# Optimization experiments

Measured on AMD Instinct MI355X. Metric: run time of the kernel, lower is better.

Reference implementation:

```python
import jax, jax.numpy as jnp
import numpy as np

B, T, NE, NZ, H = 64, 1024, 256, 64, 256  # batch, timesteps, n_e, n_z, encoder_hidden
SW_HID = 128  # switch MLP hidden width (hardcoded in source)


def setup_inputs() -> dict:
    key = jax.random.key(0)
    ks = jax.random.split(key, 16)
    s = 0.05
    p = lambda k, shape: (jax.random.normal(k, shape, dtype=jnp.float32) * s)
    return {
        "e_seq": jax.random.normal(ks[0], (B, T, NE), dtype=jnp.float32),
        "eps": jax.random.normal(ks[1], (B, T, NZ), dtype=jnp.float32),  # randn_like noise, precomputed
        # GRU forward direction (torch layout: weight_ih [3H, NE] order r,z,n)
        "w_ih_f": p(ks[2], (3 * H, NE)), "w_hh_f": p(ks[3], (3 * H, H)),
        "b_ih_f": jnp.zeros((3 * H,), jnp.float32), "b_hh_f": jnp.zeros((3 * H,), jnp.float32),
        # GRU backward direction
        "w_ih_b": p(ks[4], (3 * H, NE)), "w_hh_b": p(ks[5], (3 * H, H)),
        "b_ih_b": jnp.zeros((3 * H,), jnp.float32), "b_hh_b": jnp.zeros((3 * H,), jnp.float32),
        # mu / logvar heads over [B,T,2H]
        "mu_w": p(ks[6], (NZ, 2 * H)), "mu_b": jnp.zeros((NZ,), jnp.float32),
        "lv_w": p(ks[7], (NZ, 2 * H)), "lv_b": jnp.zeros((NZ,), jnp.float32),
        # switching unit: Linear(NE + 2H + NZ, 128) -> ReLU -> Linear(128,1) -> Sigmoid
        "sw_w1": p(ks[8], (SW_HID, NE + 2 * H + NZ)), "sw_b1": jnp.zeros((SW_HID,), jnp.float32),
        "sw_w2": p(ks[9], (1, SW_HID)), "sw_b2": jnp.zeros((1,), jnp.float32),
    }


def _gru_dir(x, w_ih, w_hh, b_ih, b_hh, reverse):
    # x: [B,T,NE]; torch GRU cell: r,z = sigmoid; n = tanh(x_n + r*(W_hn h + b_hn)); h' = (1-z)*n + z*h
    xp = jnp.einsum('btn,gn->btg', x, w_ih) + b_ih  # [B,T,3H] input projections, once
    xp = jnp.swapaxes(xp, 0, 1)  # [T,B,3H]
    h0 = jnp.zeros((x.shape[0], w_hh.shape[1]), x.dtype)

    def step(h, xpt):
        hp = h @ w_hh.T + b_hh
        xr, xz, xn = jnp.split(xpt, 3, axis=-1)
        hr, hz, hn = jnp.split(hp, 3, axis=-1)
        r = jax.nn.sigmoid(xr + hr)
        z = jax.nn.sigmoid(xz + hz)
        n = jnp.tanh(xn + r * hn)
        h_new = (1.0 - z) * n + z * h
        return h_new, h_new

    _, hs = jax.lax.scan(step, h0, xp, reverse=reverse)  # outputs time-aligned even when reversed
    return jnp.swapaxes(hs, 0, 1)  # [B,T,H]


def _forward(e_seq, eps, w_ih_f, w_hh_f, b_ih_f, b_hh_f, w_ih_b, w_hh_b, b_ih_b, b_hh_b,
             mu_w, mu_b, lv_w, lv_b, sw_w1, sw_b1, sw_w2, sw_b2):
    h_f = _gru_dir(e_seq, w_ih_f, w_hh_f, b_ih_f, b_hh_f, reverse=False)
    h_b = _gru_dir(e_seq, w_ih_b, w_hh_b, b_ih_b, b_hh_b, reverse=True)
    h_seq = jnp.concatenate([h_f, h_b], axis=-1)  # [B,T,2H]

    mu = h_seq @ mu_w.T + mu_b    # [B,T,NZ]
    lv = h_seq @ lv_w.T + lv_b    # [B,T,NZ]

    n_e = e_seq.shape[-1]
    h2 = h_seq.shape[-1]
    # split switch first-layer weight by input segments [e_t | h_t | z_prev]
    w1_e = sw_w1[:, :n_e]
    w1_h = sw_w1[:, n_e:n_e + h2]
    w1_z = sw_w1[:, n_e + h2:]
    # precompute e/h contributions for all t; only z_prev contribution is sequential
    pre = jnp.einsum('btn,kn->btk', e_seq, w1_e) + jnp.einsum('bth,kh->btk', h_seq, w1_h) + sw_b1  # [B,T,128]

    z_tilde = mu + jnp.exp(0.5 * lv) * eps                    # reparameterized sample [B,T,NZ]
    kl = (-0.5 * (1.0 + lv - mu * mu - jnp.exp(lv))).sum(-1)  # [B,T]

    def step(z_prev, inputs):
        pre_t, zt_t = inputs  # [B,128], [B,NZ]
        hid = jax.nn.relu(pre_t + z_prev @ w1_z.T)
        beta = jax.nn.sigmoid(hid @ sw_w2.T + sw_b2)[..., 0]  # [B]
        z_t = beta[:, None] * zt_t + (1.0 - beta[:, None]) * z_prev
        return z_t, (z_t, beta)

    z0 = jnp.zeros((e_seq.shape[0], mu.shape[-1]), e_seq.dtype)
    _, (zs, betas) = jax.lax.scan(step, z0, (jnp.swapaxes(pre, 0, 1), jnp.swapaxes(z_tilde, 0, 1)))
    z_seq = jnp.swapaxes(zs, 0, 1)     # [B,T,NZ]
    beta_seq = jnp.swapaxes(betas, 0, 1)  # [B,T]
    kl_loss = kl.mean()
    return z_seq, kl_loss, beta_seq


def reference(e_seq, eps, w_ih_f, w_hh_f, b_ih_f, b_hh_f, w_ih_b, w_hh_b, b_ih_b, b_hh_b,
              mu_w, mu_b, lv_w, lv_b, sw_w1, sw_b1, sw_w2, sw_b2):
    return _forward(e_seq, eps, w_ih_f, w_hh_f, b_ih_f, b_hh_f, w_ih_b, w_hh_b, b_ih_b, b_hh_b,
                    mu_w, mu_b, lv_w, lv_b, sw_w1, sw_b1, sw_w2, sw_b2)
```

## Files before the change

kernel.cpp:

```cpp
#include <hip/hip_runtime.h>
#include <cstdint>

typedef _Float16 half_t;
typedef _Float16 half2_t __attribute__((ext_vector_type(2)));
typedef _Float16 h8_t __attribute__((ext_vector_type(8)));
typedef float f4_t __attribute__((ext_vector_type(4)));
typedef unsigned int uint32;
typedef uint32 uv16 __attribute__((ext_vector_type(16)));

static constexpr int B_ = 64, T_ = 1024;

#define DEV __device__ __forceinline__

DEV float fdot2f(half2_t a, half2_t b, float c) {
#if __has_builtin(__builtin_amdgcn_fdot2)
  return __builtin_amdgcn_fdot2(a, b, c, false);
#else
  return fmaf((float)a.x, (float)b.x, fmaf((float)a.y, (float)b.y, c));
#endif
}

DEV float fast_rcp(float x) { return __builtin_amdgcn_rcpf(x); }
DEV float sigmf(float x) { return fast_rcp(1.f + __expf(-x)); }
DEV float tanhf_(float x) { return 1.f - 2.f * fast_rcp(1.f + __expf(2.f * x)); }
DEV uint32 pack2(float a, float b) {
  half2_t h; h.x = (half_t)a; h.y = (half_t)b;
  return __builtin_bit_cast(uint32, h);
}
DEV half2_t bch2(uint32 u) { return __builtin_bit_cast(half2_t, u); }

DEV void gload_lds16(const void* g, void* l) {
  __builtin_amdgcn_global_load_lds(
      (const __attribute__((address_space(1))) uint32*)g,
      (__attribute__((address_space(3))) uint32*)l, 16, 0, 0);
}

#define WSEL(va, vb, j) bch2(((j) < 16) ? (va)[(j) & 15] : (vb)[((j) - 16) & 15])

__global__ __launch_bounds__(256) void pack_w(
    const float* __restrict__ w_ih_f, const float* __restrict__ w_ih_b,
    const float* __restrict__ mu_w, const float* __restrict__ lv_w,
    const float* __restrict__ sw_w1,
    const float* __restrict__ w_hh_f, const float* __restrict__ w_hh_b,
    const float* __restrict__ b_ih_f, const float* __restrict__ b_ih_b,
    const float* __restrict__ b_hh_f, const float* __restrict__ b_hh_b,
    const float* __restrict__ mu_b, const float* __restrict__ lv_b,
    const float* __restrict__ sw_b1,
    uint32* __restrict__ wihf, uint32* __restrict__ wihb,
    uint32* __restrict__ wchf, uint32* __restrict__ wchb, uint32* __restrict__ wce2,
    uint32* __restrict__ whh, uint32* __restrict__ w1z,
    float* __restrict__ biasc, float* __restrict__ biasf, float* __restrict__ biasb) {
  int id = blockIdx.x * 256 + threadIdx.x;
  if (id < 98304) { wihf[id] = pack2(w_ih_f[2*id], w_ih_f[2*id+1]); return; }
  id -= 98304;
  if (id < 98304) { wihb[id] = pack2(w_ih_b[2*id], w_ih_b[2*id+1]); return; }
  id -= 98304;
  if (id < 32768) {
    int n = id >> 7, c0 = (id & 127) * 2;
    const float* p = (n < 64)  ? mu_w + n * 512 + c0
                   : (n < 128) ? lv_w + (n - 64) * 512 + c0
                               : sw_w1 + (n - 128) * 832 + 256 + c0;
    wchf[id] = pack2(p[0], p[1]); return;
  }
  id -= 32768;
  if (id < 32768) {
    int n = id >> 7, c0 = (id & 127) * 2;
    const float* p = (n < 64)  ? mu_w + n * 512 + 256 + c0
                   : (n < 128) ? lv_w + (n - 64) * 512 + 256 + c0
                               : sw_w1 + (n - 128) * 832 + 512 + c0;
    wchb[id] = pack2(p[0], p[1]); return;
  }
  id -= 32768;
  if (id < 16384) {
    int n = id >> 7, c0 = (id & 127) * 2;
    wce2[id] = pack2(sw_w1[n * 832 + c0], sw_w1[n * 832 + c0 + 1]); return;
  }
  id -= 16384;
  if (id < 196608) {
    int dd = id / 98304, q = id % 98304;
    int j = q >> 9, t2 = q & 511;
    int rr = t2 >> 2, pp = t2 & 3;
    int gi = j >> 5, ck = j & 31;
    int g = gi >> 1, i = gi & 1;
    int row = 256 * g + 2 * rr + i;
    int k0 = pp * 64 + 2 * ck;
    const float* w = dd ? w_hh_b : w_hh_f;
    whh[id] = pack2(w[row * 256 + k0], w[row * 256 + k0 + 1]);
    return;
  }
  id -= 196608;
  if (id < 4096) {
    int j = id >> 6, kk = id & 63;
    int row = (j < 32) ? kk : kk + 64;
    int jj = j & 31;
    w1z[id] = pack2(sw_w1[row * 832 + 768 + 2 * jj], sw_w1[row * 832 + 768 + 2 * jj + 1]);
    return;
  }
  id -= 4096;
  if (id < 256) {
    biasc[id] = (id < 64) ? mu_b[id] : (id < 128) ? lv_b[id - 64] : sw_b1[id - 128];
    return;
  }
  id -= 256;
  if (id < 768) { biasf[id] = b_ih_f[id] + (id < 512 ? b_hh_f[id] : 0.f); return; }
  id -= 768;
  if (id < 768) { biasb[id] = b_ih_b[id] + (id < 512 ? b_hh_b[id] : 0.f); return; }
}

template <int AF32, int ACC>
__global__ __launch_bounds__(256) void gemm_t(
    const void* __restrict__ Ap, int lda,
    const half_t* __restrict__ Bw,
    const float* __restrict__ bias,
    half_t* __restrict__ C, int ldc, int K) {
  __shared__ __align__(16) half_t smem[16384];
  half_t* As = smem;
  half_t* Bs = smem + 8192;
  const int tid = threadIdx.x;
  const int lane = tid & 63, w = tid >> 6;
  const int n0 = blockIdx.x * 128, m0 = blockIdx.y * 128;
  const int r8 = lane >> 3, c8 = lane & 7;
  f4_t acc[4][4];
  f4_t zero = {0.f, 0.f, 0.f, 0.f};
#pragma unroll
  for (int i = 0; i < 4; ++i)
#pragma unroll
    for (int j = 0; j < 4; ++j) acc[i][j] = zero;
  const int wm = (w >> 1) * 64, wn = (w & 1) * 64;
  for (int ks = 0; ks < K; ks += 64) {
    if constexpr (AF32) {
      const float* Af = (const float*)Ap;
#pragma unroll
      for (int it = 0; it < 4; ++it) {
        int c = it * 256 + tid;
        int row = c >> 3, coff = (c & 7) * 8;
        const float* ap = Af + (size_t)(m0 + row) * lda + ks + coff;
        float4 v0 = *(const float4*)ap;
        float4 v1 = *(const float4*)(ap + 4);
        uint4 u;
        u.x = pack2(v0.x, v0.y); u.y = pack2(v0.z, v0.w);
        u.z = pack2(v1.x, v1.y); u.w = pack2(v1.z, v1.w);
        *(uint4*)&As[(size_t)c * 8] = u;
      }
    } else {
      const half_t* Af = (const half_t*)Ap;
#pragma unroll
      for (int c = 0; c < 4; ++c) {
        int row = w * 32 + c * 8 + r8;
        gload_lds16(Af + (size_t)(m0 + row) * lda + ks + c8 * 8, As + (w * 4 + c) * 512);
      }
    }
#pragma unroll
    for (int c = 0; c < 4; ++c) {
      int row = w * 32 + c * 8 + r8;
      gload_lds16(Bw + (size_t)(n0 + row) * K + ks + c8 * 8, Bs + (w * 4 + c) * 512);
    }
    __syncthreads();
#pragma unroll
    for (int kk = 0; kk < 2; ++kk) {
      h8_t af[4], bf[4];
      const int ko = kk * 32 + (lane >> 4) * 8;
#pragma unroll
      for (int i = 0; i < 4; ++i) af[i] = *(const h8_t*)&As[(wm + i * 16 + (lane & 15)) * 64 + ko];
#pragma unroll
      for (int j = 0; j < 4; ++j) bf[j] = *(const h8_t*)&Bs[(wn + j * 16 + (lane & 15)) * 64 + ko];
#pragma unroll
      for (int i = 0; i < 4; ++i)
#pragma unroll
        for (int j = 0; j < 4; ++j)
          acc[i][j] = __builtin_amdgcn_mfma_f32_16x16x32_f16(af[i], bf[j], acc[i][j], 0, 0, 0);
    }
    __syncthreads();
  }
  const int cl4 = lane & 15, rl4 = lane >> 4;
#pragma unroll
  for (int j = 0; j < 4; ++j) {
    float bj = bias ? bias[n0 + wn + j * 16 + cl4] : 0.f;
#pragma unroll
    for (int i = 0; i < 4; ++i)
#pragma unroll
      for (int q = 0; q < 4; ++q) {
        int rl = wm + i * 16 + rl4 * 4 + q;
        int cc = wn + j * 16 + cl4;
        smem[rl * 128 + cc] = (half_t)(acc[i][j][q] + bj);
      }
  }
  __syncthreads();
#pragma unroll
  for (int it = 0; it < 8; ++it) {
    int idx = it * 256 + tid;
    int row = idx >> 4, colc = idx & 15;
    uint4 v = *(const uint4*)&smem[row * 128 + colc * 8];
    half_t* cp = C + (size_t)(m0 + row) * ldc + n0 + colc * 8;
    if constexpr (ACC) {
      uint4 o = *(const uint4*)cp;
      h8_t vv = __builtin_bit_cast(h8_t, v) + __builtin_bit_cast(h8_t, o);
      v = __builtin_bit_cast(uint4, vv);
    }
    *(uint4*)cp = v;
  }
}

__global__ __launch_bounds__(512, 2) void gru_rec(
    uint32* __restrict__ xp,
    const uint32* __restrict__ whh2,
    const float* __restrict__ bhh_f, const float* __restrict__ bhh_b) {
  const int wg = blockIdx.x;
  const int d = wg >> 6, b = wg & 63;
  const int tid = threadIdx.x;
  const int r = tid >> 2, p = tid & 3;
  __shared__ uint32 hb[2][144];
  if (tid < 144) { hb[0][tid] = 0; hb[1][tid] = 0; }
  uv16 w0a, w0b, w1a, w1b, w2a, w2b, w3a, w3b, w4a, w4b, w5a, w5b;
  {
    const uint32* wp = whh2 + (size_t)d * 98304 + tid;
#define LD16(vec, base)                                   \
  _Pragma("unroll") for (int e = 0; e < 16; ++e) vec[e] = \
      wp[(size_t)((base) + e) * 512];
    LD16(w0a, 0);   LD16(w0b, 16);  LD16(w1a, 32);  LD16(w1b, 48);
    LD16(w2a, 64);  LD16(w2b, 80);  LD16(w3a, 96);  LD16(w3b, 112);
    LD16(w4a, 128); LD16(w4b, 144); LD16(w5a, 160); LD16(w5b, 176);
#undef LD16
    asm volatile("" : "+v"(w0a), "+v"(w0b), "+v"(w1a), "+v"(w1b), "+v"(w2a), "+v"(w2b));
    asm volatile("" : "+v"(w3a), "+v"(w3b), "+v"(w4a), "+v"(w4b), "+v"(w5a), "+v"(w5b));
  }
  const float* bhh = d ? bhh_b : bhh_f;
  const float bhn0 = bhh[512 + 2 * r], bhn1 = bhh[512 + 2 * r + 1];
  uint32* xpu = xp + ((size_t)d * B_ + b) * T_ * 384;
  float h0 = 0.f, h1 = 0.f;
  const int dt = d ? -1 : 1;
  int t = d ? (T_ - 1) : 0;
  uint32 xr_n = 0, xz_n = 0, xn_n = 0;
  if (p == 0) {
    const uint32* rowp = xpu + (size_t)t * 384;
    xr_n = rowp[r]; xz_n = rowp[128 + r]; xn_n = rowp[256 + r];
  }
  const int rdbase = p * 36;
  const int wslice = (r >> 5) * 36 + (r & 31);
  __syncthreads();
  for (int step = 0; step < T_; ++step) {
    const int cur = step & 1;
    const uint32 xr = xr_n, xz = xz_n, xn = xn_n;
    const int tn = (step < T_ - 1) ? (t + dt) : t;
    if (p == 0) {
      const uint32* rowp = xpu + (size_t)tn * 384;
      xr_n = rowp[r]; xz_n = rowp[128 + r]; xn_n = rowp[256 + r];
    }
    float a00 = 0, a10 = 0, a01 = 0, a11 = 0, a02 = 0, a12 = 0;
    const uint32* hc = &hb[cur][rdbase];
#pragma unroll
    for (int c = 0; c < 4; ++c) {
      uint4 u0 = *(const uint4*)(hc + c * 8);
      uint4 u1 = *(const uint4*)(hc + c * 8 + 4);
      uint32 hv[8] = {u0.x, u0.y, u0.z, u0.w, u1.x, u1.y, u1.z, u1.w};
#pragma unroll
      for (int e = 0; e < 8; ++e) {
        const int j = c * 8 + e;
        half2_t hh = bch2(hv[e]);
        a00 = fdot2f(WSEL(w0a, w0b, j), hh, a00);
        a10 = fdot2f(WSEL(w1a, w1b, j), hh, a10);
        a01 = fdot2f(WSEL(w2a, w2b, j), hh, a01);
        a11 = fdot2f(WSEL(w3a, w3b, j), hh, a11);
        a02 = fdot2f(WSEL(w4a, w4b, j), hh, a02);
        a12 = fdot2f(WSEL(w5a, w5b, j), hh, a12);
      }
    }
    a00 += __shfl_xor(a00, 1); a00 += __shfl_xor(a00, 2);
    a10 += __shfl_xor(a10, 1); a10 += __shfl_xor(a10, 2);
    a01 += __shfl_xor(a01, 1); a01 += __shfl_xor(a01, 2);
    a11 += __shfl_xor(a11, 1); a11 += __shfl_xor(a11, 2);
    a02 += __shfl_xor(a02, 1); a02 += __shfl_xor(a02, 2);
    a12 += __shfl_xor(a12, 1); a12 += __shfl_xor(a12, 2);
    if (p == 0) {
      half2_t xrv = bch2(xr), xzv = bch2(xz), xnv = bch2(xn);
      float r0 = sigmf((float)xrv.x + a00);
      float z0 = sigmf((float)xzv.x + a01);
      float n0 = tanhf_((float)xnv.x + r0 * (a02 + bhn0));
      h0 = (1.f - z0) * n0 + z0 * h0;
      float r1 = sigmf((float)xrv.y + a10);
      float z1 = sigmf((float)xzv.y + a11);
      float n1 = tanhf_((float)xnv.y + r1 * (a12 + bhn1));
      h1 = (1.f - z1) * n1 + z1 * h1;
      uint32 ph = pack2(h0, h1);
      hb[cur ^ 1][wslice] = ph;
      xpu[(size_t)t * 384 + r] = ph;
    }
    __syncthreads();
    t = tn;
  }
}

__global__ __launch_bounds__(256) void zkl(const half_t* __restrict__ hp,
                                           const float* __restrict__ eps,
                                           float* __restrict__ ztil,
                                           float* __restrict__ klp) {
  const int blk = blockIdx.x, tid = threadIdx.x;
  const size_t bt = (size_t)blk * 4 + (tid >> 6);
  const int j = tid & 63;
  float mu = (float)hp[bt * 768 + j];
  float lv = (float)hp[bt * 768 + 64 + j];
  float ev = eps[bt * 64 + j];
  ztil[bt * 64 + j] = mu + __expf(0.5f * lv) * ev;
  float term = 1.f + lv - mu * mu - __expf(lv);
#pragma unroll
  for (int s = 1; s < 64; s <<= 1) term += __shfl_xor(term, s);
  __shared__ float red[4];
  if ((tid & 63) == 0) red[tid >> 6] = term;
  __syncthreads();
  if (tid == 0) klp[blk] = red[0] + red[1] + red[2] + red[3];
}

__global__ __launch_bounds__(256) void klred(const float* __restrict__ klp,
                                             float* __restrict__ out) {
  const int tid = threadIdx.x;
  float s = 0.f;
  for (int i = tid; i < 16384; i += 256) s += klp[i];
#pragma unroll
  for (int st = 1; st < 64; st <<= 1) s += __shfl_xor(s, st);
  __shared__ float red[4];
  if ((tid & 63) == 0) red[tid >> 6] = s;
  __syncthreads();
  if (tid == 0) out[0] = (red[0] + red[1] + red[2] + red[3]) * (-0.5f / 65536.f);
}

__global__ __launch_bounds__(64) void z_scan(
    const half_t* __restrict__ hp,
    const float* __restrict__ zt_arr,
    const uint32* __restrict__ w1z,
    const float* __restrict__ sw_w2, const float* __restrict__ sw_b2,
    float* __restrict__ z_out, float* __restrict__ beta_out) {
  const int b = blockIdx.x;
  const int k = threadIdx.x;
  uv16 z0a, z0b, z1a, z1b;
  {
#define LDZ(vec, base)                                    \
  _Pragma("unroll") for (int e = 0; e < 16; ++e) vec[e] = \
      w1z[((base) + e) * 64 + k];
    LDZ(z0a, 0); LDZ(z0b, 16); LDZ(z1a, 32); LDZ(z1b, 48);
#undef LDZ
    asm volatile("" : "+v"(z0a), "+v"(z0b), "+v"(z1a), "+v"(z1b));
  }
  const float w2k0 = sw_w2[k], w2k1 = sw_w2[k + 64], b2 = sw_b2[0];
  __shared__ uint32 zbuf[2][32];
  if (k < 32) { zbuf[0][k] = 0; zbuf[1][k] = 0; }
  __syncthreads();
  float zf = 0.f;
  const size_t bt0 = (size_t)b * T_;
  float pre0n = (float)hp[bt0 * 768 + 128 + k];
  float pre1n = (float)hp[bt0 * 768 + 192 + k];
  float ztn = zt_arr[bt0 * 64 + k];
  for (int t = 0; t < T_; ++t) {
    const int cur = t & 1;
    const float pre0 = pre0n, pre1 = pre1n, zt = ztn;
    const int tn = (t < T_ - 1) ? t + 1 : t;
    pre0n = (float)hp[(bt0 + tn) * 768 + 128 + k];
    pre1n = (float)hp[(bt0 + tn) * 768 + 192 + k];
    ztn = zt_arr[(bt0 + tn) * 64 + k];
    float a0 = 0, a1 = 0, a2 = 0, a3 = 0;
#pragma unroll
    for (int q = 0; q < 8; ++q) {
      uint4 u = *(const uint4*)&zbuf[cur][q * 4];
      const int m = q * 4;
      a0 = fdot2f(WSEL(z0a, z0b, m),     bch2(u.x), a0);
      a1 = fdot2f(WSEL(z0a, z0b, m + 1), bch2(u.y), a1);
      a0 = fdot2f(WSEL(z0a, z0b, m + 2), bch2(u.z), a0);
      a1 = fdot2f(WSEL(z0a, z0b, m + 3), bch2(u.w), a1);
      a2 = fdot2f(WSEL(z1a, z1b, m),     bch2(u.x), a2);
      a3 = fdot2f(WSEL(z1a, z1b, m + 1), bch2(u.y), a3);
      a2 = fdot2f(WSEL(z1a, z1b, m + 2), bch2(u.z), a2);
      a3 = fdot2f(WSEL(z1a, z1b, m + 3), bch2(u.w), a3);
    }
    float hid0 = fmaxf(pre0 + a0 + a1, 0.f);
    float hid1 = fmaxf(pre1 + a2 + a3, 0.f);
    float v = fmaf(hid0, w2k0, hid1 * w2k1);
#pragma unroll
    for (int s = 1; s < 64; s <<= 1) v += __shfl_xor(v, s);
    const float beta = sigmf(v + b2);
    zf = beta * zt + (1.f - beta) * zf;
    z_out[(bt0 + t) * 64 + k] = zf;
    if (k == 0) beta_out[bt0 + t] = beta;
    float zo = __shfl_xor(zf, 1);
    if ((k & 1) == 0) zbuf[cur ^ 1][k >> 1] = pack2(zf, zo);
    asm volatile("s_waitcnt lgkmcnt(0)" ::: "memory");
  }
}

extern "C" void kernel_launch(void* const* d_in, const int* in_sizes, int n_in,
                              void* d_out, int out_size, void* d_ws, size_t ws_size,
                              hipStream_t stream) {
  (void)in_sizes; (void)n_in; (void)out_size;
  const float* e_seq  = (const float*)d_in[0];
  const float* eps    = (const float*)d_in[1];
  const float* w_ih_f = (const float*)d_in[2];
  const float* w_hh_f = (const float*)d_in[3];
  const float* b_ih_f = (const float*)d_in[4];
  const float* b_hh_f = (const float*)d_in[5];
  const float* w_ih_b = (const float*)d_in[6];
  const float* w_hh_b = (const float*)d_in[7];
  const float* b_ih_b = (const float*)d_in[8];
  const float* b_hh_b = (const float*)d_in[9];
  const float* mu_w   = (const float*)d_in[10];
  const float* mu_b   = (const float*)d_in[11];
  const float* lv_w   = (const float*)d_in[12];
  const float* lv_b   = (const float*)d_in[13];
  const float* sw_w1  = (const float*)d_in[14];
  const float* sw_b1  = (const float*)d_in[15];
  const float* sw_w2  = (const float*)d_in[16];
  const float* sw_b2  = (const float*)d_in[17];

  const size_t NEED = 201326592 + 1924096;
  if (ws_size < NEED) return;
  char* ws = (char*)d_ws;
  half_t* xpf = (half_t*)ws;
  half_t* xpb = (half_t*)(ws + 100663296);
  half_t* hp  = xpf + 512;
  float*  ztil = (float*)(ws + 100663296);
  float*  klp  = (float*)(ws + 100663296 + 16777216);
  char* wr = ws + 201326592;
  uint32* wihf  = (uint32*)(wr);
  uint32* wihb  = (uint32*)(wr + 393216);
  uint32* wchf  = (uint32*)(wr + 786432);
  uint32* wchb  = (uint32*)(wr + 917504);
  uint32* wce2  = (uint32*)(wr + 1048576);
  uint32* whh2  = (uint32*)(wr + 1114112);
  uint32* w1z2  = (uint32*)(wr + 1900544);
  float*  biasc = (float*)(wr + 1916928);
  float*  biasf = (float*)(wr + 1917952);
  float*  biasb = (float*)(wr + 1921024);

  pack_w<<<1879, 256, 0, stream>>>(w_ih_f, w_ih_b, mu_w, lv_w, sw_w1, w_hh_f, w_hh_b,
                                   b_ih_f, b_ih_b, b_hh_f, b_hh_b, mu_b, lv_b, sw_b1,
                                   wihf, wihb, wchf, wchb, wce2, whh2, w1z2,
                                   biasc, biasf, biasb);
  gemm_t<1, 0><<<dim3(6, 512), 256, 0, stream>>>(e_seq, 256, (const half_t*)wihf, biasf, xpf, 768, 256);
  gemm_t<1, 0><<<dim3(6, 512), 256, 0, stream>>>(e_seq, 256, (const half_t*)wihb, biasb, xpb, 768, 256);
  gru_rec<<<128, 512, 0, stream>>>((uint32*)ws, whh2, b_hh_f, b_hh_b);
  gemm_t<0, 0><<<dim3(2, 512), 256, 0, stream>>>(xpf, 768, (const half_t*)wchf, biasc, hp, 768, 256);
  gemm_t<0, 1><<<dim3(2, 512), 256, 0, stream>>>(xpb, 768, (const half_t*)wchb, nullptr, hp, 768, 256);
  gemm_t<1, 1><<<dim3(1, 512), 256, 0, stream>>>(e_seq, 256, (const half_t*)wce2, nullptr, hp + 128, 768, 256);
  zkl<<<16384, 256, 0, stream>>>(hp, eps, ztil, klp);
  klred<<<1, 256, 0, stream>>>(klp, (float*)d_out + 4194304);
  z_scan<<<64, 64, 0, stream>>>(hp, ztil, w1z2, sw_w2, sw_b2, (float*)d_out, (float*)d_out + 4194305);
}
```

Before: 2.105 ms.

## Split GRU recurrence across 1024 threads with 8-way K split and staged x inputs

The GRU recurrent kernel now uses 1024 threads per block, splitting each hidden pair's dot product 8 ways instead of 4. That halves the per-thread register-held weights to 96 dwords and shortens the serial dot chain per step. The per-step input projections are prefetched cooperatively into a double-buffered shared array instead of per-lane registers, and the weight packing layout changes to match. The cost is an extra shuffle stage, a larger block sync each step, and changed register limits (z_scan also drops its asm register pin and adds an occupancy hint).

```diff
diff --git a/kernel.cpp b/kernel.cpp
--- a/kernel.cpp
+++ b/kernel.cpp
@@ -78,12 +78,12 @@
   id -= 16384;
   if (id < 196608) {
     int dd = id / 98304, q = id % 98304;
-    int j = q >> 9, t2 = q & 511;
-    int rr = t2 >> 2, pp = t2 & 3;
-    int gi = j >> 5, ck = j & 31;
-    int g = gi >> 1, i = gi & 1;
-    int row = 256 * g + 2 * rr + i;
-    int k0 = pp * 64 + 2 * ck;
+    int j = q >> 10, t2 = q & 1023;
+    int g = j >> 4, e = j & 15;
+    int rr = t2 >> 3, pp = t2 & 7;
+    int gi = g >> 1, i = g & 1;
+    int row = 256 * gi + 2 * rr + i;
+    int k0 = 2 * (pp * 16 + e);
     const float* w = dd ? w_hh_b : w_hh_f;
     whh[id] = pack2(w[row * 256 + k0], w[row * 256 + k0 + 1]);
     return;
@@ -201,28 +201,23 @@
   }
 }
 
-__global__ __launch_bounds__(512, 2) void gru_rec(
+__global__ __launch_bounds__(1024, 4) void gru_rec(
     uint32* __restrict__ xp,
-    const uint32* __restrict__ whh2,
+    const uint32* __restrict__ whh3,
     const float* __restrict__ bhh_f, const float* __restrict__ bhh_b) {
   const int wg = blockIdx.x;
   const int d = wg >> 6, b = wg & 63;
   const int tid = threadIdx.x;
-  const int r = tid >> 2, p = tid & 3;
-  __shared__ uint32 hb[2][144];
-  if (tid < 144) { hb[0][tid] = 0; hb[1][tid] = 0; }
-  uv16 w0a, w0b, w1a, w1b, w2a, w2b, w3a, w3b, w4a, w4b, w5a, w5b;
+  const int r = tid >> 3, p = tid & 7;
+  __shared__ uint32 hb[2][160];
+  __shared__ uint32 xbuf[2][384];
+  if (tid < 160) { hb[0][tid] = 0; }
+  uv16 w0, w1, w2, w3, w4, w5;
   {
-    const uint32* wp = whh2 + (size_t)d * 98304 + tid;
-#define LD16(vec, base)                                   \
-  _Pragma("unroll") for (int e = 0; e < 16; ++e) vec[e] = \
-      wp[(size_t)((base) + e) * 512];
-    LD16(w0a, 0);   LD16(w0b, 16);  LD16(w1a, 32);  LD16(w1b, 48);
-    LD16(w2a, 64);  LD16(w2b, 80);  LD16(w3a, 96);  LD16(w3b, 112);
-    LD16(w4a, 128); LD16(w4b, 144); LD16(w5a, 160); LD16(w5b, 176);
-#undef LD16
-    asm volatile("" : "+v"(w0a), "+v"(w0b), "+v"(w1a), "+v"(w1b), "+v"(w2a), "+v"(w2b));
-    asm volatile("" : "+v"(w3a), "+v"(w3b), "+v"(w4a), "+v"(w4b), "+v"(w5a), "+v"(w5b));
+    const uint32* wp = whh3 + (size_t)d * 98304 + tid;
+#define LDW(vec, g) _Pragma("unroll") for (int e = 0; e < 16; ++e) vec[e] = wp[((g) * 16 + e) * 1024];
+    LDW(w0, 0) LDW(w1, 1) LDW(w2, 2) LDW(w3, 3) LDW(w4, 4) LDW(w5, 5)
+#undef LDW
   }
   const float* bhh = d ? bhh_b : bhh_f;
   const float bhn0 = bhh[512 + 2 * r], bhn1 = bhh[512 + 2 * r + 1];
@@ -230,61 +225,56 @@
   float h0 = 0.f, h1 = 0.f;
   const int dt = d ? -1 : 1;
   int t = d ? (T_ - 1) : 0;
-  uint32 xr_n = 0, xz_n = 0, xn_n = 0;
-  if (p == 0) {
-    const uint32* rowp = xpu + (size_t)t * 384;
-    xr_n = rowp[r]; xz_n = rowp[128 + r]; xn_n = rowp[256 + r];
-  }
-  const int rdbase = p * 36;
-  const int wslice = (r >> 5) * 36 + (r & 31);
+  if (tid < 384) xbuf[0][tid] = xpu[(size_t)t * 384 + tid];
   __syncthreads();
   for (int step = 0; step < T_; ++step) {
     const int cur = step & 1;
-    const uint32 xr = xr_n, xz = xz_n, xn = xn_n;
     const int tn = (step < T_ - 1) ? (t + dt) : t;
+    uint32 xv = 0;
+    if (tid < 384) xv = xpu[(size_t)tn * 384 + tid];
+    float a0 = 0, a1 = 0, a2 = 0, a3 = 0, a4 = 0, a5 = 0;
+    const uint32* hc = &hb[cur][p * 20];
+#pragma unroll
+    for (int c = 0; c < 4; ++c) {
+      uint4 u = *(const uint4*)(hc + c * 4);
+      half2_t g0 = bch2(u.x), g1 = bch2(u.y), g2 = bch2(u.z), g3 = bch2(u.w);
+      const int e = c * 4;
+      a0 = fdot2f(bch2(w0[e]), g0, a0); a0 = fdot2f(bch2(w0[e + 1]), g1, a0);
+      a0 = fdot2f(bch2(w0[e + 2]), g2, a0); a0 = fdot2f(bch2(w0[e + 3]), g3, a0);
+      a1 = fdot2f(bch2(w1[e]), g0, a1); a1 = fdot2f(bch2(w1[e + 1]), g1, a1);
+      a1 = fdot2f(bch2(w1[e + 2]), g2, a1); a1 = fdot2f(bch2(w1[e + 3]), g3, a1);
+      a2 = fdot2f(bch2(w2[e]), g0, a2); a2 = fdot2f(bch2(w2[e + 1]), g1, a2);
+      a2 = fdot2f(bch2(w2[e + 2]), g2, a2); a2 = fdot2f(bch2(w2[e + 3]), g3, a2);
+      a3 = fdot2f(bch2(w3[e]), g0, a3); a3 = fdot2f(bch2(w3[e + 1]), g1, a3);
+      a3 = fdot2f(bch2(w3[e + 2]), g2, a3); a3 = fdot2f(bch2(w3[e + 3]), g3, a3);
+      a4 = fdot2f(bch2(w4[e]), g0, a4); a4 = fdot2f(bch2(w4[e + 1]), g1, a4);
+      a4 = fdot2f(bch2(w4[e + 2]), g2, a4); a4 = fdot2f(bch2(w4[e + 3]), g3, a4);
+      a5 = fdot2f(bch2(w5[e]), g0, a5); a5 = fdot2f(bch2(w5[e + 1]), g1, a5);
+      a5 = fdot2f(bch2(w5[e + 2]), g2, a5); a5 = fdot2f(bch2(w5[e + 3]), g3, a5);
+    }
+    a0 += __shfl_xor(a0, 1); a0 += __shfl_xor(a0, 2); a0 += __shfl_xor(a0, 4);
+    a1 += __shfl_xor(a1, 1); a1 += __shfl_xor(a1, 2); a1 += __shfl_xor(a1, 4);
+    a2 += __shfl_xor(a2, 1); a2 += __shfl_xor(a2, 2); a2 += __shfl_xor(a2, 4);
+    a3 += __shfl_xor(a3, 1); a3 += __shfl_xor(a3, 2); a3 += __shfl_xor(a3, 4);
+    a4 += __shfl_xor(a4, 1); a4 += __shfl_xor(a4, 2); a4 += __shfl_xor(a4, 4);
+    a5 += __shfl_xor(a5, 1); a5 += __shfl_xor(a5, 2); a5 += __shfl_xor(a5, 4);
     if (p == 0) {
-      const uint32* rowp = xpu + (size_t)tn * 384;
-      xr_n = rowp[r]; xz_n = rowp[128 + r]; xn_n = rowp[256 + r];
-    }
-    float a00 = 0, a10 = 0, a01 = 0, a11 = 0, a02 = 0, a12 = 0;
-    const uint32* hc = &hb[cur][rdbase];
-#pragma unroll
-    for (int c = 0; c < 4; ++c) {
-      uint4 u0 = *(const uint4*)(hc + c * 8);
-      uint4 u1 = *(const uint4*)(hc + c * 8 + 4);
-      uint32 hv[8] = {u0.x, u0.y, u0.z, u0.w, u1.x, u1.y, u1.z, u1.w};
-#pragma unroll
-      for (int e = 0; e < 8; ++e) {
-        const int j = c * 8 + e;
-        half2_t hh = bch2(hv[e]);
-        a00 = fdot2f(WSEL(w0a, w0b, j), hh, a00);
-        a10 = fdot2f(WSEL(w1a, w1b, j), hh, a10);
-        a01 = fdot2f(WSEL(w2a, w2b, j), hh, a01);
-        a11 = fdot2f(WSEL(w3a, w3b, j), hh, a11);
-        a02 = fdot2f(WSEL(w4a, w4b, j), hh, a02);
-        a12 = fdot2f(WSEL(w5a, w5b, j), hh, a12);
-      }
-    }
-    a00 += __shfl_xor(a00, 1); a00 += __shfl_xor(a00, 2);
-    a10 += __shfl_xor(a10, 1); a10 += __shfl_xor(a10, 2);
-    a01 += __shfl_xor(a01, 1); a01 += __shfl_xor(a01, 2);
-    a11 += __shfl_xor(a11, 1); a11 += __shfl_xor(a11, 2);
-    a02 += __shfl_xor(a02, 1); a02 += __shfl_xor(a02, 2);
-    a12 += __shfl_xor(a12, 1); a12 += __shfl_xor(a12, 2);
-    if (p == 0) {
-      half2_t xrv = bch2(xr), xzv = bch2(xz), xnv = bch2(xn);
-      float r0 = sigmf((float)xrv.x + a00);
-      float z0 = sigmf((float)xzv.x + a01);
-      float n0 = tanhf_((float)xnv.x + r0 * (a02 + bhn0));
+      half2_t xrv = bch2(xbuf[cur][r]);
+      half2_t xzv = bch2(xbuf[cur][128 + r]);
+      half2_t xnv = bch2(xbuf[cur][256 + r]);
+      float r0 = sigmf((float)xrv.x + a0);
+      float r1 = sigmf((float)xrv.y + a1);
+      float z0 = sigmf((float)xzv.x + a2);
+      float z1 = sigmf((float)xzv.y + a3);
+      float n0 = tanhf_((float)xnv.x + r0 * (a4 + bhn0));
+      float n1 = tanhf_((float)xnv.y + r1 * (a5 + bhn1));
       h0 = (1.f - z0) * n0 + z0 * h0;
-      float r1 = sigmf((float)xrv.y + a10);
-      float z1 = sigmf((float)xzv.y + a11);
-      float n1 = tanhf_((float)xnv.y + r1 * (a12 + bhn1));
       h1 = (1.f - z1) * n1 + z1 * h1;
       uint32 ph = pack2(h0, h1);
-      hb[cur ^ 1][wslice] = ph;
+      hb[cur ^ 1][(r >> 4) * 20 + (r & 15)] = ph;
       xpu[(size_t)t * 384 + r] = ph;
     }
+    if (tid < 384) xbuf[cur ^ 1][tid] = xv;
     __syncthreads();
     t = tn;
   }
@@ -323,7 +313,7 @@
   if (tid == 0) out[0] = (red[0] + red[1] + red[2] + red[3]) * (-0.5f / 65536.f);
 }
 
-__global__ __launch_bounds__(64) void z_scan(
+__global__ __launch_bounds__(64, 4) void z_scan(
     const half_t* __restrict__ hp,
     const float* __restrict__ zt_arr,
     const uint32* __restrict__ w1z,
@@ -338,7 +328,6 @@
       w1z[((base) + e) * 64 + k];
     LDZ(z0a, 0); LDZ(z0b, 16); LDZ(z1a, 32); LDZ(z1b, 48);
 #undef LDZ
-    asm volatile("" : "+v"(z0a), "+v"(z0b), "+v"(z1a), "+v"(z1b));
   }
   const float w2k0 = sw_w2[k], w2k1 = sw_w2[k + 64], b2 = sw_b2[0];
   __shared__ uint32 zbuf[2][32];
@@ -422,7 +411,7 @@
   uint32* wchf  = (uint32*)(wr + 786432);
   uint32* wchb  = (uint32*)(wr + 917504);
   uint32* wce2  = (uint32*)(wr + 1048576);
-  uint32* whh2  = (uint32*)(wr + 1114112);
+  uint32* whh3  = (uint32*)(wr + 1114112);
   uint32* w1z2  = (uint32*)(wr + 1900544);
   float*  biasc = (float*)(wr + 1916928);
   float*  biasf = (float*)(wr + 1917952);
@@ -430,11 +419,11 @@
 
   pack_w<<<1879, 256, 0, stream>>>(w_ih_f, w_ih_b, mu_w, lv_w, sw_w1, w_hh_f, w_hh_b,
                                    b_ih_f, b_ih_b, b_hh_f, b_hh_b, mu_b, lv_b, sw_b1,
-                                   wihf, wihb, wchf, wchb, wce2, whh2, w1z2,
+                                   wihf, wihb, wchf, wchb, wce2, whh3, w1z2,
                                    biasc, biasf, biasb);
   gemm_t<1, 0><<<dim3(6, 512), 256, 0, stream>>>(e_seq, 256, (const half_t*)wihf, biasf, xpf, 768, 256);
   gemm_t<1, 0><<<dim3(6, 512), 256, 0, stream>>>(e_seq, 256, (const half_t*)wihb, biasb, xpb, 768, 256);
-  gru_rec<<<128, 512, 0, stream>>>((uint32*)ws, whh2, b_hh_f, b_hh_b);
+  gru_rec<<<128, 1024, 0, stream>>>((uint32*)ws, whh3, b_hh_f, b_hh_b);
   gemm_t<0, 0><<<dim3(2, 512), 256, 0, stream>>>(xpf, 768, (const half_t*)wchf, biasc, hp, 768, 256);
   gemm_t<0, 1><<<dim3(2, 512), 256, 0, stream>>>(xpb, 768, (const half_t*)wchb, nullptr, hp, 768, 256);
   gemm_t<1, 1><<<dim3(1, 512), 256, 0, stream>>>(e_seq, 256, (const half_t*)wce2, nullptr, hp + 128, 768, 256);
```

Result: slower. 2.477 ms (+17.7%).
